# Optimization experiments

Measured on AMD Instinct MI355X. Metric: run time of the kernel, lower is better.

The kernel has to match this reference:

```python
import jax, jax.numpy as jnp
import numpy as np
import math

B, L, H = 32, 2048, 8
DMET, SDIM = 16, 27
DM, NL, DS, TE = 256, 4, 64, 256
LT = L + H - 1
DT_MIN, DT_MAX = 1e-3, 0.1


def setup_inputs() -> dict:
    key = jax.random.key(0)
    ks = jax.random.split(key, 24)
    inp = {
        'x_past': jax.random.normal(ks[0], (B, L, DMET), jnp.float32),
        'noisy_future': jax.random.normal(ks[1], (B, H, 1), jnp.float32),
        't': jax.random.uniform(ks[2], (B,), jnp.float32),
        'x_future': jax.random.normal(ks[3], (B, H - 1, DMET), jnp.float32),
        'static_attr': jax.random.normal(ks[4], (B, 1, SDIM), jnp.float32),
        # MPFourier buffers
        'freqs': 2 * math.pi * jax.random.normal(ks[5], (TE,), jnp.float32),
        'phases': 2 * math.pi * jax.random.uniform(ks[6], (TE,), jnp.float32),
        # input projection (d_met+1+static_dim -> d_model)
        'in_W': jax.random.normal(ks[7], (DMET + 1 + SDIM, DM), jnp.float32) / np.sqrt(DMET + 1 + SDIM),
        'in_b': jnp.zeros((DM,), jnp.float32),
        # time MLP
        'tm_W1': jax.random.normal(ks[8], (TE, 2 * TE), jnp.float32) / np.sqrt(TE),
        'tm_b1': jnp.zeros((2 * TE,), jnp.float32),
        'tm_W2': jax.random.normal(ks[9], (2 * TE, DM), jnp.float32) / np.sqrt(2 * TE),
        'tm_b2': jnp.zeros((DM,), jnp.float32),
        # stacked S4D (LTI) block params, leading dim = n_layers
        'log_dt': jax.random.uniform(ks[10], (NL, DM), jnp.float32) * (math.log(DT_MAX) - math.log(DT_MIN)) + math.log(DT_MIN),
        'A_re': -0.5 * jnp.ones((NL, DM, DS), jnp.float32),
        'A_im': math.pi * jnp.broadcast_to(jnp.arange(DS, dtype=jnp.float32), (NL, DM, DS)),
        'C_re': jax.random.normal(ks[11], (NL, DM, DS), jnp.float32) * (0.5 ** 0.5),
        'C_im': jax.random.normal(ks[12], (NL, DM, DS), jnp.float32) * (0.5 ** 0.5),
        'D': jax.random.normal(ks[13], (NL, DM), jnp.float32),
        'out_W': jax.random.normal(ks[14], (NL, DM, 2 * DM), jnp.float32) / np.sqrt(DM),
        'out_b': jnp.zeros((NL, 2 * DM), jnp.float32),
        # batchnorm
        'bn_gamma': jnp.ones((NL, DM), jnp.float32),
        'bn_beta': jnp.zeros((NL, DM), jnp.float32),
        # head
        'head_W1': jax.random.normal(ks[15], (DM, DM // 2), jnp.float32) / np.sqrt(DM),
        'head_b1': jnp.zeros((DM // 2,), jnp.float32),
        'head_W2': jax.random.normal(ks[16], (DM // 2, 1), jnp.float32) / np.sqrt(DM // 2),
        'head_b2': jnp.zeros((1,), jnp.float32),
    }
    return inp


def _ssm_block(u, log_dt, A_re, A_im, C_re, C_im, D, out_W, out_b):
    # u: [B, d, Lc]. S4D-style diagonal SSM via FFT causal convolution.
    Lc = u.shape[-1]
    dt = jnp.exp(log_dt)                                 # [d]
    A = A_re + 1j * A_im                                 # [d, n], Re(A) < 0
    dtA = dt[:, None] * A                                # [d, n]
    Ck = (C_re + 1j * C_im) * jnp.expm1(dtA) / A         # ZOH-style discretized C
    van = jnp.exp(dtA[:, :, None] * jnp.arange(Lc))      # [d, n, Lc] Vandermonde
    K = 2.0 * jnp.einsum('dn,dnl->dl', Ck, van).real     # [d, Lc]
    nfft = 2 * Lc
    y = jnp.fft.irfft(jnp.fft.rfft(u, nfft) * jnp.fft.rfft(K, nfft)[None], nfft)[..., :Lc]
    y = jax.nn.gelu(y + D[None, :, None] * u)
    z = jnp.einsum('bdl,de->bel', y, out_W) + out_b[None, :, None]  # [B, 2d, Lc]
    z1, z2 = jnp.split(z, 2, axis=1)
    return z1 * jax.nn.sigmoid(z2)                       # GLU


def _batchnorm1d(h, gamma, beta):
    # h: [B, d, Lc]; training-mode batch statistics, eps matches torch default.
    mean = h.mean(axis=(0, 2), keepdims=True)
    var = ((h - mean) ** 2).mean(axis=(0, 2), keepdims=True)
    return (h - mean) * jax.lax.rsqrt(var + 1e-5) * gamma[None, :, None] + beta[None, :, None]


def reference(x_past, noisy_future, t, x_future, static_attr,
              freqs, phases, in_W, in_b, tm_W1, tm_b1, tm_W2, tm_b2,
              log_dt, A_re, A_im, C_re, C_im, D, out_W, out_b,
              bn_gamma, bn_beta, head_W1, head_b1, head_W2, head_b2):
    Bc = x_past.shape[0]
    # MPFourier time features
    t_feats = jnp.cos(t[:, None] * freqs[None, :] + phases[None, :]) * math.sqrt(2)
    t_b = jax.nn.silu(t_feats @ tm_W1 + tm_b1) @ tm_W2 + tm_b2     # [B, DM]
    # feature fusion
    all_met = jnp.concatenate([x_past, x_future], axis=1)          # [B, LT, DMET]
    all_flow = jnp.concatenate([jnp.zeros((Bc, L - 1, 1), x_past.dtype), noisy_future], axis=1)
    static_seq = jnp.broadcast_to(static_attr[:, :1, :], (Bc, LT, SDIM))
    feats = jnp.concatenate([all_met, all_flow, static_seq], axis=-1)
    h = feats @ in_W + in_b                                        # [B, LT, DM]
    h = h.at[:, L - 1:, :].add(t_b[:, None, :])                    # time_full conditioning
    h = jnp.transpose(h, (0, 2, 1))                                # [B, DM, LT]
    for i in range(NL):
        z = _ssm_block(h, log_dt[i], A_re[i], A_im[i], C_re[i], C_im[i],
                       D[i], out_W[i], out_b[i])
        h = _batchnorm1d(h + z, bn_gamma[i], bn_beta[i])           # dropout = identity (eval)
    h = jnp.transpose(h, (0, 2, 1))                                # [B, LT, DM]
    out = jax.nn.silu(h @ head_W1 + head_b1) @ head_W2 + head_b2   # [B, LT, 1]
    return out[:, -H:, :]
```

## Files before the change

### kernel.cpp

```cpp
#include <hip/hip_runtime.h>
#include <hip/hip_bf16.h>
#include <math.h>

#define B_   32
#define L_   2048
#define H_   8
#define DMET 16
#define SDIM 27
#define DM   256
#define NL   4
#define DS   64
#define TE   256
#define LT   2055
#define LTR  2176
#define TCH  128
#define NC   17
#define COLS 544
#define NTOT (B_ * LT)

typedef __attribute__((ext_vector_type(8))) short short8;
typedef __attribute__((ext_vector_type(4))) short short4v;
typedef __attribute__((ext_vector_type(4))) float floatx4;

__device__ __forceinline__ float sigmoidf_(float x) {
    float e = __builtin_amdgcn_exp2f(-1.4426950408889634f * x);
    return __builtin_amdgcn_rcpf(1.0f + e);
}

__device__ __forceinline__ float gelu_tanh(float x) {
    float inner = 1.5957691216057308f * fmaf(0.044715f * x * x, x, x);
    return x * sigmoidf_(inner);
}

__device__ __forceinline__ short bfs(float x) {
    __hip_bfloat16 h = __float2bfloat16(x);
    return *(short*)&h;
}

__device__ __forceinline__ float sbf(short s) {
    unsigned u = ((unsigned)(unsigned short)s) << 16;
    return __uint_as_float(u);
}

__device__ __forceinline__ void glds16(const void* g, void* l) {
    __builtin_amdgcn_global_load_lds(
        (const __attribute__((address_space(1))) unsigned*)g,
        (__attribute__((address_space(3))) unsigned*)l, 16, 0, 0);
}

__global__ __launch_bounds__(256) void time_mlp_kernel(
    const float* __restrict__ t, const float* __restrict__ freqs,
    const float* __restrict__ phases,
    const float* __restrict__ W1, const float* __restrict__ b1,
    const float* __restrict__ W2, const float* __restrict__ b2,
    float* __restrict__ tb) {
    int b = blockIdx.x;
    int tid = threadIdx.x;
    __shared__ float f[TE];
    __shared__ float hid[2 * TE];
    float tv = t[b];
    f[tid] = cosf(fmaf(tv, freqs[tid], phases[tid])) * 1.4142135623730951f;
    __syncthreads();
    float a0 = b1[tid], a1 = b1[tid + TE];
    for (int k = 0; k < TE; ++k) {
        float fk = f[k];
        a0 = fmaf(fk, W1[k * 2 * TE + tid], a0);
        a1 = fmaf(fk, W1[k * 2 * TE + tid + TE], a1);
    }
    hid[tid]      = a0 * sigmoidf_(a0);
    hid[tid + TE] = a1 * sigmoidf_(a1);
    __syncthreads();
    float acc = b2[tid];
    for (int j = 0; j < 2 * TE; ++j)
        acc = fmaf(hid[j], W2[j * DM + tid], acc);
    tb[b * DM + tid] = acc;
}

__global__ __launch_bounds__(256) void wt_prep_kernel(
    const float* __restrict__ out_W, __hip_bfloat16* __restrict__ Wtp) {
    int bid = blockIdx.x;
    int layer = bid >> 8, k = bid & 255;
    int e = threadIdx.x;
    const float* src = out_W + ((size_t)layer * 256 + k) * 512;
    #pragma unroll
    for (int q = 0; q < 2; ++q) {
        int ee = e + q * 256;
        int P = ee & 255, half = ee >> 8;
        int by = P >> 6, pp = P & 63;
        int g = pp >> 5;
        int tcol = (pp & 31) + half * 32;
        int c = by * 128 + g * 64 + tcol;
        Wtp[((size_t)layer * 512 + c) * 256 + k] = __float2bfloat16(src[ee]);
    }
}

__global__ __launch_bounds__(256) void input_proj_kernel(
    const float* __restrict__ xp, const float* __restrict__ nf,
    const float* __restrict__ xf, const float* __restrict__ sa,
    const float* __restrict__ inW, const float* __restrict__ inb,
    const float* __restrict__ tb, __hip_bfloat16* __restrict__ Ub) {
    int b  = blockIdx.y;
    int l0 = blockIdx.x * 256;
    int tx = threadIdx.x;
    int l  = l0 + tx;

    __shared__ float feats[256][18];
    __shared__ float Ws[17][DM];
    __shared__ float sdot[DM];
    __shared__ float tbs[DM];
    __shared__ float sstat[SDIM];

    if (tx < SDIM) sstat[tx] = sa[b * SDIM + tx];
    for (int k = 0; k < 17; ++k) Ws[k][tx] = inW[k * DM + tx];
    tbs[tx] = tb[b * DM + tx];

    bool valid = (l < LT);
    if (valid) {
        const float* src = (l < L_) ? &xp[((size_t)b * L_ + l) * DMET]
                                    : &xf[((size_t)b * (H_ - 1) + (l - L_)) * DMET];
        #pragma unroll
        for (int k = 0; k < DMET; ++k) feats[tx][k] = src[k];
        feats[tx][16] = (l >= L_ - 1) ? nf[b * H_ + (l - (L_ - 1))] : 0.0f;
    }
    __syncthreads();

    float sd = 0.0f;
    for (int k = 0; k < SDIM; ++k)
        sd = fmaf(sstat[k], inW[(17 + k) * DM + tx], sd);
    sdot[tx] = sd;
    __syncthreads();

    if (l >= LTR) return;
    size_t baseb = ((size_t)b * DM) * LTR + l;
    if (!valid) {
        __hip_bfloat16 z = __float2bfloat16(0.0f);
        for (int d = 0; d < DM; ++d) Ub[baseb + (size_t)d * LTR] = z;
        return;
    }
    bool cond = (l >= L_ - 1);
    for (int d = 0; d < DM; ++d) {
        float acc = inb[d] + sdot[d] + (cond ? tbs[d] : 0.0f);
        #pragma unroll
        for (int k = 0; k < 17; ++k)
            acc = fmaf(feats[tx][k], Ws[k][d], acc);
        Ub[baseb + (size_t)d * LTR] = __float2bfloat16(acc);
    }
}

__global__ __launch_bounds__(256) void prep_kernel(
    const float* __restrict__ log_dt,
    const float* __restrict__ A_re, const float* __restrict__ A_im,
    const float* __restrict__ C_re, const float* __restrict__ C_im,
    const float* __restrict__ Dp,
    const float* __restrict__ gamma, const float* __restrict__ beta,
    float* __restrict__ stats, float* __restrict__ scsh,
    __hip_bfloat16* __restrict__ Abig, __hip_bfloat16* __restrict__ SA,
    float* __restrict__ Rsh, float* __restrict__ T1sh, int layer) {
    int d = blockIdx.x;
    int t = threadIdx.x;
    __shared__ float sAr[64], sAi[64], sCkr[64], sCki[64];
    __shared__ float kap[TCH];
    __shared__ float csum[TCH];
    __shared__ float s_sc, s_sh;

    if (t == 0) {
        float sc, sh;
        if (layer == 0) { sc = 1.0f; sh = 0.0f; }
        else {
            float s = stats[d], q = stats[DM + d];
            float mean = s * (1.0f / NTOT);
            float var  = q * (1.0f / NTOT) - mean * mean;
            sc = rsqrtf(var + 1e-5f) * gamma[(layer - 1) * DM + d];
            sh = beta[(layer - 1) * DM + d] - mean * sc;
        }
        s_sc = sc; s_sh = sh;
        scsh[d] = sc; scsh[DM + d] = sh;
        stats[d] = 0.0f; stats[DM + d] = 0.0f;
    }
    __syncthreads();
    float sc = s_sc, sh = s_sh;

    float dt = expf(log_dt[layer * DM + d]);
    float Dd = Dp[layer * DM + d];
    if (t < 64) {
        size_t ab = ((size_t)layer * DM + d) * DS + t;
        float Ar = A_re[ab], Ai = A_im[ab], Cr = C_re[ab], Ci = C_im[ab];
        float ar = dt * Ar, ai = dt * Ai;
        float e = expf(ar);
        float wre = e * cosf(ai), wim = e * sinf(ai);
        float mr = wre - 1.0f, mi = wim;
        float den = 1.0f / (Ar * Ar + Ai * Ai);
        float qr = (mr * Ar + mi * Ai) * den, qi = (mi * Ar - mr * Ai) * den;
        sCkr[t] = Cr * qr - Ci * qi;
        sCki[t] = Cr * qi + Ci * qr;
        sAr[t] = ar;
        sAi[t] = ai;
        float s2 = sinf(0.5f * ai);
        float dr = fmaf(expm1f(ar), cosf(ai), -2.0f * s2 * s2);
        float di = e * sinf(ai);
        float a128 = 128.0f * ar, b128 = 128.0f * ai;
        float s2b = sinf(0.5f * b128);
        float nr = fmaf(expm1f(a128), cosf(b128), -2.0f * s2b * s2b);
        float ni = expf(a128) * sinf(b128);
        float dd2 = 1.0f / (dr * dr + di * di);
        float gr = (nr * dr + ni * di) * dd2;
        float gi = (ni * dr - nr * di) * dd2;
        Rsh[(size_t)d * 128 + t]      = sh * gr;
        Rsh[(size_t)d * 128 + 64 + t] = sh * gi;
    }
    __syncthreads();

    {
        int delta = t >> 1, half = t & 1;
        float fd = (float)delta;
        float p = 0.0f;
        #pragma unroll 8
        for (int n = half * 32; n < half * 32 + 32; ++n) {
            float er = expf(fd * sAr[n]);
            float ph = fd * sAi[n];
            p += er * (sCkr[n] * cosf(ph) - sCki[n] * sinf(ph));
        }
        p += __shfl_xor(p, 1);
        if (half == 0) kap[delta] = 2.0f * p + (delta == 0 ? Dd : 0.0f);
    }
    __syncthreads();

    if (t < 128) csum[t] = kap[t];
    __syncthreads();
    for (int off = 1; off < 128; off <<= 1) {
        float v = 0.0f;
        if (t >= off && t < 128) v = csum[t - off];
        __syncthreads();
        if (t < 128) csum[t] += v;
        __syncthreads();
    }
    if (t < 128) T1sh[(size_t)d * 128 + t] = sh * csum[t];

    __hip_bfloat16* Ad = Abig + (size_t)d * TCH * 256;
    for (int idx = t; idx < TCH * TCH; idx += 256) {
        int i = idx >> 7, m = idx & 127;
        Ad[(size_t)i * 256 + m] = __float2bfloat16(m <= i ? sc * kap[i - m] : 0.0f);
    }
    for (int idx = t; idx < TCH * 64; idx += 256) {
        int i = idx >> 6, n = idx & 63;
        float fp = (float)(i + 1);
        float er = expf(fp * sAr[n]);
        float ph = fp * sAi[n];
        float c = cosf(ph), s = sinf(ph);
        float vr = er * (sCkr[n] * c - sCki[n] * s);
        float vi = er * (sCkr[n] * s + sCki[n] * c);
        Ad[(size_t)i * 256 + 128 + n] = __float2bfloat16(2.0f * vr);
        Ad[(size_t)i * 256 + 192 + n] = __float2bfloat16(-2.0f * vi);
    }
    __hip_bfloat16* Sd = SA + (size_t)d * TCH * TCH;
    for (int idx = t; idx < 64 * TCH; idx += 256) {
        int n = idx >> 7, m = idx & 127;
        float fp = (float)(127 - m);
        float er = sc * expf(fp * sAr[n]);
        float ph = fp * sAi[n];
        Sd[(size_t)n * 128 + m]        = __float2bfloat16(er * cosf(ph));
        Sd[(size_t)(64 + n) * 128 + m] = __float2bfloat16(er * sinf(ph));
    }
}

__global__ __launch_bounds__(256) void sgemm_kernel(
    const __hip_bfloat16* __restrict__ Ub, const __hip_bfloat16* __restrict__ SA,
    const float* __restrict__ Rsh, __hip_bfloat16* __restrict__ S) {
    int id = blockIdx.x;
    int xcd = id & 7, j = id >> 3;
    int d = xcd * 32 + ((j * 7282) >> 16);
    int cb = j - ((j * 7282) >> 16) * 9;
    int tid = threadIdx.x, wave = tid >> 6, lane = tid & 63;
    int lm = lane & 15, quad = lane >> 4;
    const __hip_bfloat16* SAd = SA + (size_t)d * TCH * TCH;

    __shared__ short Bs[8192];

    short8 a0r[4], a1r[4];
    #pragma unroll
    for (int kk = 0; kk < 4; ++kk) {
        a0r[kk] = *(const short8*)(SAd + (size_t)(wave * 32 + lm) * TCH + kk * 32 + quad * 8);
        a1r[kk] = *(const short8*)(SAd + (size_t)(wave * 32 + 16 + lm) * TCH + kk * 32 + quad * 8);
    }

    #pragma unroll
    for (int it = 0; it < 4; ++it) {
        int idx = it * 256 + tid;
        int kk = idx >> 8;
        int nt = (idx >> 6) & 3;
        int q  = (idx >> 4) & 3;
        int cc = idx & 15;
        int col = cb * 64 + nt * 16 + cc;
        int colc = col < COLS ? col : COLS - 1;
        int bh = (colc * 241) >> 12;
        int c = colc - bh * 17;
        const __hip_bfloat16* src =
            Ub + ((size_t)bh * DM + d) * LTR + (size_t)c * TCH + kk * 32 + q * 8;
        glds16(src, (char*)Bs + idx * 16);
    }

    floatx4 acc[2][4];
    floatx4 zf = {0.f, 0.f, 0.f, 0.f};
    #pragma unroll
    for (int mi = 0; mi < 2; ++mi)
        #pragma unroll
        for (int nt = 0; nt < 4; ++nt) acc[mi][nt] = zf;

    asm volatile("s_waitcnt vmcnt(2)" ::: "memory");
    __builtin_amdgcn_s_barrier();
    asm volatile("" ::: "memory");

    #pragma unroll
    for (int kk = 0; kk < 2; ++kk) {
        #pragma unroll
        for (int nt = 0; nt < 4; ++nt) {
            short8 bv = *(const short8*)(Bs + kk * 2048 + nt * 512 + lane * 8);
            acc[0][nt] = __builtin_amdgcn_mfma_f32_16x16x32_bf16(a0r[kk], bv, acc[0][nt], 0, 0, 0);
            acc[1][nt] = __builtin_amdgcn_mfma_f32_16x16x32_bf16(a1r[kk], bv, acc[1][nt], 0, 0, 0);
        }
    }

    asm volatile("s_waitcnt vmcnt(0)" ::: "memory");
    __builtin_amdgcn_s_barrier();
    asm volatile("" ::: "memory");

    #pragma unroll
    for (int kk = 2; kk < 4; ++kk) {
        #pragma unroll
        for (int nt = 0; nt < 4; ++nt) {
            short8 bv = *(const short8*)(Bs + kk * 2048 + nt * 512 + lane * 8);
            acc[0][nt] = __builtin_amdgcn_mfma_f32_16x16x32_bf16(a0r[kk], bv, acc[0][nt], 0, 0, 0);
            acc[1][nt] = __builtin_amdgcn_mfma_f32_16x16x32_bf16(a1r[kk], bv, acc[1][nt], 0, 0, 0);
        }
    }

    #pragma unroll
    for (int mi = 0; mi < 2; ++mi) {
        int row = wave * 32 + mi * 16 + quad * 4;
        float4 rs = *(const float4*)(Rsh + (size_t)d * 128 + row);
        #pragma unroll
        for (int nt = 0; nt < 4; ++nt) {
            int col = cb * 64 + nt * 16 + lm;
            if (col >= COLS) continue;
            short4v o;
            o[0] = bfs(acc[mi][nt][0] + rs.x); o[1] = bfs(acc[mi][nt][1] + rs.y);
            o[2] = bfs(acc[mi][nt][2] + rs.z); o[3] = bfs(acc[mi][nt][3] + rs.w);
            *(short4v*)(S + ((size_t)d * COLS + col) * TCH + row) = o;
        }
    }
}

__global__ __launch_bounds__(64) void carry_kernel(
    __hip_bfloat16* __restrict__ SX,
    const float* __restrict__ log_dt,
    const float* __restrict__ A_re, const float* __restrict__ A_im,
    int layer) {
    int d = blockIdx.x, b = blockIdx.y;
    int n = threadIdx.x;
    float dt = expf(log_dt[layer * DM + d]);
    size_t ab = ((size_t)layer * DM + d) * DS + n;
    float Ar = A_re[ab], Ai = A_im[ab];
    float e = expf(dt * Ar);
    float wre = e * cosf(dt * Ai), wim = e * sinf(dt * Ai);
    #pragma unroll
    for (int t = 0; t < 7; ++t) {
        float r = wre * wre - wim * wim;
        wim = 2.0f * wre * wim; wre = r;
    }
    size_t base = ((size_t)d * COLS + (size_t)b * NC) * TCH + n;
    float sre[NC], sim[NC];
    #pragma unroll
    for (int c = 0; c < NC; ++c) {
        sre[c] = __bfloat162float(SX[base + (size_t)c * TCH]);
        sim[c] = __bfloat162float(SX[base + (size_t)c * TCH + 64]);
    }
    float xr = 0.0f, xi = 0.0f;
    #pragma unroll
    for (int c = 0; c < NC; ++c) {
        SX[base + (size_t)c * TCH]      = __float2bfloat16(xr);
        SX[base + (size_t)c * TCH + 64] = __float2bfloat16(xi);
        float nr = wre * xr - wim * xi + sre[c];
        xi = wre * xi + wim * xr + sim[c];
        xr = nr;
    }
}

__global__ __launch_bounds__(256) void mainscan_kernel(
    const __hip_bfloat16* __restrict__ Ub, const __hip_bfloat16* __restrict__ X,
    const __hip_bfloat16* __restrict__ Abig, const float* __restrict__ T1sh,
    __hip_bfloat16* __restrict__ Ybt) {
    int id = blockIdx.x;
    int xcd = id & 7, j = id >> 3;
    int d = xcd * 32 + ((j * 7282) >> 16);
    int cb = j - ((j * 7282) >> 16) * 9;
    int tid = threadIdx.x, wave = tid >> 6, lane = tid & 63;
    int lm = lane & 15, quad = lane >> 4;
    const __hip_bfloat16* Ad = Abig + (size_t)d * TCH * 256;

    __shared__ short Bs[16384];

    short8 a0r[8], a1r[8];
    #pragma unroll
    for (int kk = 0; kk < 8; ++kk) {
        a0r[kk] = *(const short8*)(Ad + (size_t)(wave * 32 + lm) * 256 + kk * 32 + quad * 8);
        a1r[kk] = *(const short8*)(Ad + (size_t)(wave * 32 + 16 + lm) * 256 + kk * 32 + quad * 8);
    }

    #pragma unroll
    for (int it = 0; it < 8; ++it) {
        int idx = it * 256 + tid;
        int kk = idx >> 8;
        int nt = (idx >> 6) & 3;
        int q  = (idx >> 4) & 3;
        int cc = idx & 15;
        int col = cb * 64 + nt * 16 + cc;
        int colc = col < COLS ? col : COLS - 1;
        int bh = (colc * 241) >> 12;
        int c = colc - bh * 17;
        const __hip_bfloat16* src;
        if (kk < 4)
            src = Ub + ((size_t)bh * DM + d) * LTR + (size_t)c * TCH + kk * 32 + q * 8;
        else
            src = X + ((size_t)d * COLS + colc) * TCH + (kk - 4) * 32 + q * 8;
        glds16(src, (char*)Bs + idx * 16);
    }

    floatx4 acc[2][4];
    floatx4 zf = {0.f, 0.f, 0.f, 0.f};
    #pragma unroll
    for (int mi = 0; mi < 2; ++mi)
        #pragma unroll
        for (int nt = 0; nt < 4; ++nt) acc[mi][nt] = zf;

    asm volatile("s_waitcnt vmcnt(4)" ::: "memory");
    __builtin_amdgcn_s_barrier();
    asm volatile("" ::: "memory");

    #pragma unroll
    for (int kk = 0; kk < 4; ++kk) {
        #pragma unroll
        for (int nt = 0; nt < 4; ++nt) {
            short8 bv = *(const short8*)(Bs + kk * 2048 + nt * 512 + lane * 8);
            acc[0][nt] = __builtin_amdgcn_mfma_f32_16x16x32_bf16(a0r[kk], bv, acc[0][nt], 0, 0, 0);
            acc[1][nt] = __builtin_amdgcn_mfma_f32_16x16x32_bf16(a1r[kk], bv, acc[1][nt], 0, 0, 0);
        }
    }

    asm volatile("s_waitcnt vmcnt(0)" ::: "memory");
    __builtin_amdgcn_s_barrier();
    asm volatile("" ::: "memory");

    #pragma unroll
    for (int kk = 4; kk < 8; ++kk) {
        #pragma unroll
        for (int nt = 0; nt < 4; ++nt) {
            short8 bv = *(const short8*)(Bs + kk * 2048 + nt * 512 + lane * 8);
            acc[0][nt] = __builtin_amdgcn_mfma_f32_16x16x32_bf16(a0r[kk], bv, acc[0][nt], 0, 0, 0);
            acc[1][nt] = __builtin_amdgcn_mfma_f32_16x16x32_bf16(a1r[kk], bv, acc[1][nt], 0, 0, 0);
        }
    }

    #pragma unroll
    for (int mi = 0; mi < 2; ++mi) {
        int row0 = wave * 32 + mi * 16 + quad * 4;
        float4 t1 = *(const float4*)(T1sh + (size_t)d * 128 + row0);
        #pragma unroll
        for (int nt = 0; nt < 4; ++nt) {
            int col = cb * 64 + nt * 16 + lm;
            if (col >= COLS) continue;
            int bh = (col * 241) >> 12;
            int c = col - bh * 17;
            int l0 = c * TCH + row0;
            float g0 = gelu_tanh(acc[mi][nt][0] + t1.x);
            float g1 = gelu_tanh(acc[mi][nt][1] + t1.y);
            float g2 = gelu_tanh(acc[mi][nt][2] + t1.z);
            float g3 = gelu_tanh(acc[mi][nt][3] + t1.w);
            __hip_bfloat16* dst = Ybt + ((size_t)bh * DM + d) * LTR + l0;
            if (l0 + 3 < LT) {
                short4v o;
                o[0] = bfs(g0); o[1] = bfs(g1); o[2] = bfs(g2); o[3] = bfs(g3);
                *(short4v*)dst = o;
            } else {
                if (l0 + 0 < LT) dst[0] = __float2bfloat16(g0);
                if (l0 + 1 < LT) dst[1] = __float2bfloat16(g1);
                if (l0 + 2 < LT) dst[2] = __float2bfloat16(g2);
                if (l0 + 3 < LT) dst[3] = __float2bfloat16(g3);
            }
        }
    }
}

__global__ __launch_bounds__(256) void gemm_glu_mfma_kernel(
    const __hip_bfloat16* __restrict__ Ybt, __hip_bfloat16* __restrict__ Ub,
    const __hip_bfloat16* __restrict__ Wtp, const float* __restrict__ out_b,
    const float* __restrict__ scsh, float* __restrict__ stats, int layer) {
    int id = blockIdx.x;
    int r8 = id & 7, j = id >> 3;
    int by = r8 >> 1;
    int sub = (r8 & 1) * 272 + j;
    int bq = (sub * 3856) >> 16;
    int bx = sub - bq * 17;
    int b = bq;
    int tid = threadIdx.x;
    int wave = tid >> 6, lane = tid & 63;
    int lm = lane & 15, quad = lane >> 4;
    int l0 = bx * 128;

    __shared__ short lds[16384];

    const __hip_bfloat16* Wl = Wtp + (size_t)layer * 512 * 256 + (size_t)by * 128 * 256;

    int kp = tid >> 4;
    int l8 = tid & 15;
    const __hip_bfloat16* srcA = Ybt + ((size_t)b * DM + 2 * kp) * LTR + l0 + l8 * 8;
    int woff[8];
    {
        int qA = kp >> 2;
        #pragma unroll
        for (int jj = 0; jj < 8; ++jj) {
            int lloc = l8 * 8 + jj;
            int s4 = (qA + lloc + l8) & 3;
            woff[jj] = lloc * 32 + s4 * 8 + (kp & 3) * 2;
        }
    }
    int rB_[2], qB_[2];
    #pragma unroll
    for (int i = 0; i < 2; ++i) {
        int u = i * 256 + tid;
        int r = u >> 2;
        rB_[i] = r;
        qB_[i] = ((u & 3) - r - (r >> 3)) & 3;
    }
    int aoff[4], boff[4];
    #pragma unroll
    for (int mi = 0; mi < 4; ++mi) {
        int r = (wave >> 1) * 64 + mi * 16 + lm;
        aoff[mi] = r * 32 + ((quad + r + (r >> 3)) & 3) * 8;
    }
    #pragma unroll
    for (int ni = 0; ni < 4; ++ni) {
        int r = (wave & 1) * 64 + ni * 16 + lm;
        boff[ni] = r * 32 + ((quad + r + (r >> 3)) & 3) * 8;
    }

    floatx4 acc[4][4];
    floatx4 zf = {0.f, 0.f, 0.f, 0.f};
    #pragma unroll
    for (int mi = 0; mi < 4; ++mi)
        #pragma unroll
        for (int ni = 0; ni < 4; ++ni) acc[mi][ni] = zf;

#define STAGE_B(S, P)                                                         \
    {                                                                         \
        char* bb_ = (char*)(lds + (P) * 8192 + 4096);                         \
        _Pragma("unroll")                                                     \
        for (int i_ = 0; i_ < 2; ++i_)                                        \
            glds16(Wl + (size_t)rB_[i_] * 256 + (S) * 32 + qB_[i_] * 8,       \
                   bb_ + (i_ * 256 + tid) * 16);                              \
    }
#define LOAD_A(S, G0, G1)                                                     \
    {                                                                         \
        const __hip_bfloat16* pa_ = srcA + (size_t)(S) * 32 * LTR;            \
        G0 = *(const short8*)pa_;                                             \
        G1 = *(const short8*)(pa_ + LTR);                                     \
    }
#define WRITE_A(P, G0, G1)                                                    \
    {                                                                         \
        short* ab_ = lds + (P) * 8192;                                        \
        _Pragma("unroll")                                                     \
        for (int j_ = 0; j_ < 8; ++j_) {                                      \
            unsigned pk_ = (unsigned)(unsigned short)G0[j_] |                 \
                           ((unsigned)(unsigned short)G1[j_] << 16);          \
            *(unsigned*)(ab_ + woff[j_]) = pk_;                               \
        }                                                                     \
    }
#define COMPUTE(P)                                                            \
    {                                                                         \
        const short* ab_ = lds + (P) * 8192;                                  \
        const short* bb_ = ab_ + 4096;                                        \
        short8 af_[4], bf_[4];                                                \
        _Pragma("unroll")                                                     \
        for (int mi_ = 0; mi_ < 4; ++mi_)                                     \
            af_[mi_] = *(const short8*)(ab_ + aoff[mi_]);                     \
        _Pragma("unroll")                                                     \
        for (int ni_ = 0; ni_ < 4; ++ni_)                                     \
            bf_[ni_] = *(const short8*)(bb_ + boff[ni_]);                     \
        _Pragma("unroll")                                                     \
        for (int mi_ = 0; mi_ < 4; ++mi_)                                     \
            _Pragma("unroll")                                                 \
            for (int ni_ = 0; ni_ < 4; ++ni_)                                 \
                acc[mi_][ni_] = __builtin_amdgcn_mfma_f32_16x16x32_bf16(      \
                    af_[mi_], bf_[ni_], acc[mi_][ni_], 0, 0, 0);              \
    }
#define FENCE2                                                                \
    asm volatile("s_waitcnt vmcnt(2)" ::: "memory");                          \
    asm volatile("s_waitcnt lgkmcnt(0)" ::: "memory");                        \
    __builtin_amdgcn_sched_barrier(0);                                        \
    __builtin_amdgcn_s_barrier();
#define FENCE0                                                                \
    asm volatile("s_waitcnt vmcnt(0)" ::: "memory");                          \
    asm volatile("s_waitcnt lgkmcnt(0)" ::: "memory");                        \
    __builtin_amdgcn_sched_barrier(0);                                        \
    __builtin_amdgcn_s_barrier();

    short8 gE0, gE1, gO0, gO1;
    STAGE_B(0, 0);
    LOAD_A(0, gE0, gE1);
    WRITE_A(0, gE0, gE1);
    LOAD_A(1, gO0, gO1);
    asm volatile("s_waitcnt lgkmcnt(0)" ::: "memory");
    __builtin_amdgcn_sched_barrier(0);
    __builtin_amdgcn_s_barrier();

    STAGE_B(1, 1); COMPUTE(0); WRITE_A(1, gO0, gO1); LOAD_A(2, gE0, gE1); FENCE2;
    STAGE_B(2, 0); COMPUTE(1); WRITE_A(0, gE0, gE1); LOAD_A(3, gO0, gO1); FENCE2;
    STAGE_B(3, 1); COMPUTE(0); WRITE_A(1, gO0, gO1); LOAD_A(4, gE0, gE1); FENCE2;
    STAGE_B(4, 0); COMPUTE(1); WRITE_A(0, gE0, gE1); LOAD_A(5, gO0, gO1); FENCE2;
    STAGE_B(5, 1); COMPUTE(0); WRITE_A(1, gO0, gO1); LOAD_A(6, gE0, gE1); FENCE2;
    STAGE_B(6, 0); COMPUTE(1); WRITE_A(0, gE0, gE1); LOAD_A(7, gO0, gO1); FENCE2;
    STAGE_B(7, 1); COMPUTE(0); WRITE_A(1, gO0, gO1); FENCE0;
    COMPUTE(1);

#undef STAGE_B
#undef LOAD_A
#undef WRITE_A
#undef COMPUTE
#undef FENCE2
#undef FENCE0

    const float* bl = out_b + layer * 512;
    int Pbase = by * 64 + (wave & 1) * 32;
    int lw = l0 + (wave >> 1) * 64;
    #pragma unroll
    for (int ni = 0; ni < 2; ++ni) {
        int P = Pbase + ni * 16 + lm;
        float bz1 = bl[P], bz2 = bl[256 + P];
        float scP = scsh[P], shP = scsh[DM + P];
        __hip_bfloat16* ubrow = Ub + ((size_t)b * DM + P) * LTR;
        float sp = 0.f, sq = 0.f;
        #pragma unroll
        for (int mi = 0; mi < 4; ++mi) {
            int l0q = lw + mi * 16 + quad * 4;
            if (l0q >= LT) continue;
            floatx4 z1 = acc[mi][ni];
            floatx4 z2 = acc[mi][ni + 2];
            if (l0q + 4 <= LT) {
                short4v uv = *(const short4v*)(ubrow + l0q);
                float h0 = fmaf(scP, sbf(uv[0]), shP) + (z1[0] + bz1) * sigmoidf_(z2[0] + bz2);
                float h1 = fmaf(scP, sbf(uv[1]), shP) + (z1[1] + bz1) * sigmoidf_(z2[1] + bz2);
                float h2 = fmaf(scP, sbf(uv[2]), shP) + (z1[2] + bz1) * sigmoidf_(z2[2] + bz2);
                float h3 = fmaf(scP, sbf(uv[3]), shP) + (z1[3] + bz1) * sigmoidf_(z2[3] + bz2);
                short4v ov;
                ov[0] = bfs(h0); ov[1] = bfs(h1); ov[2] = bfs(h2); ov[3] = bfs(h3);
                *(short4v*)(ubrow + l0q) = ov;
                sp += (h0 + h1) + (h2 + h3);
                sq += (h0 * h0 + h1 * h1) + (h2 * h2 + h3 * h3);
            } else {
                #pragma unroll
                for (int r = 0; r < 4; ++r) {
                    int l = l0q + r;
                    if (l < LT) {
                        float uvv = __bfloat162float(ubrow[l]);
                        float hh = fmaf(scP, uvv, shP) + (z1[r] + bz1) * sigmoidf_(z2[r] + bz2);
                        ubrow[l] = __float2bfloat16(hh);
                        sp += hh; sq += hh * hh;
                    }
                }
            }
        }
        sp += __shfl_xor(sp, 16); sp += __shfl_xor(sp, 32);
        sq += __shfl_xor(sq, 16); sq += __shfl_xor(sq, 32);
        if (quad == 0) {
            atomicAdd(&stats[P], sp);
            atomicAdd(&stats[DM + P], sq);
        }
    }
}

__global__ __launch_bounds__(256) void statsfin_kernel(
    const float* __restrict__ stats,
    const float* __restrict__ gamma, const float* __restrict__ beta,
    float* __restrict__ scsh, int layer) {
    int d = threadIdx.x;
    float s = stats[d], q = stats[DM + d];
    float mean = s * (1.0f / NTOT);
    float var  = q * (1.0f / NTOT) - mean * mean;
    float sc = rsqrtf(var + 1e-5f) * gamma[layer * DM + d];
    scsh[d] = sc;
    scsh[DM + d] = beta[layer * DM + d] - mean * sc;
}

__global__ __launch_bounds__(128) void head_kernel(
    const __hip_bfloat16* __restrict__ Ub, const float* __restrict__ scsh,
    const float* __restrict__ W1, const float* __restrict__ b1,
    const float* __restrict__ W2, const float* __restrict__ b2,
    float* __restrict__ out) {
    int hh = blockIdx.x;
    int b  = blockIdx.y;
    int j  = threadIdx.x;
    int l  = (L_ - 1) + hh;
    const __hip_bfloat16* urow = Ub + ((size_t)b * DM) * LTR + l;
    float a = b1[j];
    for (int k = 0; k < DM; ++k) {
        float hn = fmaf(scsh[k], __bfloat162float(urow[(size_t)k * LTR]), scsh[DM + k]);
        a = fmaf(hn, W1[k * 128 + j], a);
    }
    float hs = a * sigmoidf_(a);
    float v = hs * W2[j];
    v += __shfl_xor(v, 1);
    v += __shfl_xor(v, 2);
    v += __shfl_xor(v, 4);
    v += __shfl_xor(v, 8);
    v += __shfl_xor(v, 16);
    v += __shfl_xor(v, 32);
    __shared__ float partial[2];
    if ((j & 63) == 0) partial[j >> 6] = v;
    __syncthreads();
    if (j == 0) out[b * H_ + hh] = partial[0] + partial[1] + b2[0];
}

extern "C" void kernel_launch(void* const* d_in, const int* in_sizes, int n_in,
                              void* d_out, int out_size, void* d_ws, size_t ws_size,
                              hipStream_t stream) {
    (void)in_sizes; (void)n_in; (void)out_size; (void)ws_size;
    const float* x_past      = (const float*)d_in[0];
    const float* noisy       = (const float*)d_in[1];
    const float* t_in        = (const float*)d_in[2];
    const float* x_future    = (const float*)d_in[3];
    const float* static_attr = (const float*)d_in[4];
    const float* freqs       = (const float*)d_in[5];
    const float* phases      = (const float*)d_in[6];
    const float* in_W        = (const float*)d_in[7];
    const float* in_b        = (const float*)d_in[8];
    const float* tm_W1       = (const float*)d_in[9];
    const float* tm_b1       = (const float*)d_in[10];
    const float* tm_W2       = (const float*)d_in[11];
    const float* tm_b2       = (const float*)d_in[12];
    const float* log_dt      = (const float*)d_in[13];
    const float* A_re        = (const float*)d_in[14];
    const float* A_im        = (const float*)d_in[15];
    const float* C_re        = (const float*)d_in[16];
    const float* C_im        = (const float*)d_in[17];
    const float* Dp          = (const float*)d_in[18];
    const float* out_W       = (const float*)d_in[19];
    const float* out_b       = (const float*)d_in[20];
    const float* bn_gamma    = (const float*)d_in[21];
    const float* bn_beta     = (const float*)d_in[22];
    const float* head_W1     = (const float*)d_in[23];
    const float* head_b1     = (const float*)d_in[24];
    const float* head_W2     = (const float*)d_in[25];
    const float* head_b2     = (const float*)d_in[26];

    char* ws = (char*)d_ws;
    const size_t UB_OFF = 1u << 20;
    const size_t UB_BYT = (size_t)B_ * DM * LTR * 2;
    const size_t R1_OFF = UB_OFF + UB_BYT;
    const size_t RB     = (size_t)256 * COLS * TCH * 2;
    const size_t R2_OFF = R1_OFF + RB;
    const size_t AB_OFF = R2_OFF + RB;
    const size_t AB_BYT = (size_t)256 * TCH * 256 * 2;
    const size_t SA_OFF = AB_OFF + AB_BYT;
    const size_t SA_BYT = (size_t)256 * TCH * TCH * 2;
    const size_t WT_OFF = SA_OFF + SA_BYT;

    float*          tb    = (float*)(ws);
    float*          stats = (float*)(ws + (64 << 10));
    float*          scsh  = (float*)(ws + (96 << 10));
    float*          Rsh   = (float*)(ws + (128 << 10));
    float*          T1sh  = (float*)(ws + (256 << 10));
    __hip_bfloat16* Ub    = (__hip_bfloat16*)(ws + UB_OFF);
    __hip_bfloat16* R1    = (__hip_bfloat16*)(ws + R1_OFF);
    __hip_bfloat16* Ybt   = (__hip_bfloat16*)(ws + R2_OFF);
    __hip_bfloat16* Abig  = (__hip_bfloat16*)(ws + AB_OFF);
    __hip_bfloat16* SA    = (__hip_bfloat16*)(ws + SA_OFF);
    __hip_bfloat16* Wtp   = (__hip_bfloat16*)(ws + WT_OFF);

    time_mlp_kernel<<<dim3(B_), 256, 0, stream>>>(
        t_in, freqs, phases, tm_W1, tm_b1, tm_W2, tm_b2, tb);

    wt_prep_kernel<<<dim3(NL * 256), 256, 0, stream>>>(out_W, Wtp);

    input_proj_kernel<<<dim3(9, B_), 256, 0, stream>>>(
        x_past, noisy, x_future, static_attr, in_W, in_b, tb, Ub);

    for (int layer = 0; layer < NL; ++layer) {
        prep_kernel<<<dim3(256), 256, 0, stream>>>(
            log_dt, A_re, A_im, C_re, C_im, Dp, bn_gamma, bn_beta,
            stats, scsh, Abig, SA, Rsh, T1sh, layer);
        sgemm_kernel<<<dim3(2304), 256, 0, stream>>>(Ub, SA, Rsh, R1);
        carry_kernel<<<dim3(256, B_), 64, 0, stream>>>(
            R1, log_dt, A_re, A_im, layer);
        mainscan_kernel<<<dim3(2304), 256, 0, stream>>>(Ub, R1, Abig, T1sh, Ybt);
        gemm_glu_mfma_kernel<<<dim3(2176), 256, 0, stream>>>(
            Ybt, Ub, Wtp, out_b, scsh, stats, layer);
    }

    statsfin_kernel<<<dim3(1), 256, 0, stream>>>(
        stats, bn_gamma, bn_beta, scsh, NL - 1);

    head_kernel<<<dim3(H_, B_), 128, 0, stream>>>(
        Ub, scsh, head_W1, head_b1, head_W2, head_b2, (float*)d_out);
}
```

Baseline: 840.5 us.

## Process three column tiles per block with pipelined LDS staging in scan GEMMs

sgemm and mainscan now have each block handle three 64-column tiles instead of one, cutting the grid from 2304 to 768 blocks. The register-resident A fragments are reused across the three tiles, and a triple-buffered LDS ring lets the global-to-LDS loads for the next tile overlap the MFMA work and epilogue of the current one. The prep kernel also switches to hardware exp2/sin/cos intrinsics with manual range reduction, which is less accurate than the libm calls. More LDS per block and fewer blocks may lower occupancy and parallelism across the CUs.

```diff
diff --git a/kernel.cpp b/kernel.cpp
--- a/kernel.cpp
+++ b/kernel.cpp
@@ -32,6 +32,20 @@
     return x * sigmoidf_(inner);
 }
 
+__device__ __forceinline__ float fexp_(float x) {
+    return __builtin_amdgcn_exp2f(1.4426950408889634f * x);
+}
+__device__ __forceinline__ float fsin_(float ph) {
+    float r = ph * 0.15915494309189535f;
+    r = r - floorf(r);
+    return __builtin_amdgcn_sinf(r);
+}
+__device__ __forceinline__ float fcos_(float ph) {
+    float r = ph * 0.15915494309189535f;
+    r = r - floorf(r);
+    return __builtin_amdgcn_cosf(r);
+}
+
 __device__ __forceinline__ short bfs(float x) {
     __hip_bfloat16 h = __float2bfloat16(x);
     return *(short*)&h;
@@ -47,6 +61,12 @@
         (const __attribute__((address_space(1))) unsigned*)g,
         (__attribute__((address_space(3))) unsigned*)l, 16, 0, 0);
 }
+
+#define BARV(n) do {                                                          \
+    asm volatile("s_waitcnt vmcnt(" #n ") lgkmcnt(0)" ::: "memory");          \
+    __builtin_amdgcn_s_barrier();                                             \
+    asm volatile("" ::: "memory");                                            \
+} while (0)
 
 __global__ __launch_bounds__(256) void time_mlp_kernel(
     const float* __restrict__ t, const float* __restrict__ freqs,
@@ -216,9 +236,9 @@
         float p = 0.0f;
         #pragma unroll 8
         for (int n = half * 32; n < half * 32 + 32; ++n) {
-            float er = expf(fd * sAr[n]);
+            float er = fexp_(fd * sAr[n]);
             float ph = fd * sAi[n];
-            p += er * (sCkr[n] * cosf(ph) - sCki[n] * sinf(ph));
+            p += er * (sCkr[n] * fcos_(ph) - sCki[n] * fsin_(ph));
         }
         p += __shfl_xor(p, 1);
         if (half == 0) kap[delta] = 2.0f * p + (delta == 0 ? Dd : 0.0f);
@@ -244,9 +264,9 @@
     for (int idx = t; idx < TCH * 64; idx += 256) {
         int i = idx >> 6, n = idx & 63;
         float fp = (float)(i + 1);
-        float er = expf(fp * sAr[n]);
+        float er = fexp_(fp * sAr[n]);
         float ph = fp * sAi[n];
-        float c = cosf(ph), s = sinf(ph);
+        float c = fcos_(ph), s = fsin_(ph);
         float vr = er * (sCkr[n] * c - sCki[n] * s);
         float vi = er * (sCkr[n] * s + sCki[n] * c);
         Ad[(size_t)i * 256 + 128 + n] = __float2bfloat16(2.0f * vr);
@@ -256,10 +276,10 @@
     for (int idx = t; idx < 64 * TCH; idx += 256) {
         int n = idx >> 7, m = idx & 127;
         float fp = (float)(127 - m);
-        float er = sc * expf(fp * sAr[n]);
+        float er = sc * fexp_(fp * sAr[n]);
         float ph = fp * sAi[n];
-        Sd[(size_t)n * 128 + m]        = __float2bfloat16(er * cosf(ph));
-        Sd[(size_t)(64 + n) * 128 + m] = __float2bfloat16(er * sinf(ph));
+        Sd[(size_t)n * 128 + m]        = __float2bfloat16(er * fcos_(ph));
+        Sd[(size_t)(64 + n) * 128 + m] = __float2bfloat16(er * fsin_(ph));
     }
 }
 
@@ -268,13 +288,14 @@
     const float* __restrict__ Rsh, __hip_bfloat16* __restrict__ S) {
     int id = blockIdx.x;
     int xcd = id & 7, j = id >> 3;
-    int d = xcd * 32 + ((j * 7282) >> 16);
-    int cb = j - ((j * 7282) >> 16) * 9;
+    int dj = (j * 21846) >> 16;
+    int d = xcd * 32 + dj;
+    int g = j - dj * 3;
     int tid = threadIdx.x, wave = tid >> 6, lane = tid & 63;
     int lm = lane & 15, quad = lane >> 4;
     const __hip_bfloat16* SAd = SA + (size_t)d * TCH * TCH;
 
-    __shared__ short Bs[8192];
+    __shared__ short Bs[12288];
 
     short8 a0r[4], a1r[4];
     #pragma unroll
@@ -283,21 +304,19 @@
         a1r[kk] = *(const short8*)(SAd + (size_t)(wave * 32 + 16 + lm) * TCH + kk * 32 + quad * 8);
     }
 
-    #pragma unroll
-    for (int it = 0; it < 4; ++it) {
-        int idx = it * 256 + tid;
-        int kk = idx >> 8;
-        int nt = (idx >> 6) & 3;
-        int q  = (idx >> 4) & 3;
-        int cc = idx & 15;
-        int col = cb * 64 + nt * 16 + cc;
+    int ntS = (tid >> 6) & 3, qS = (tid >> 4) & 3, ccS = tid & 15;
+    const __hip_bfloat16* srcB[3];
+    #pragma unroll
+    for (int t = 0; t < 3; ++t) {
+        int col = (3 * g + t) * 64 + ntS * 16 + ccS;
         int colc = col < COLS ? col : COLS - 1;
         int bh = (colc * 241) >> 12;
         int c = colc - bh * 17;
-        const __hip_bfloat16* src =
-            Ub + ((size_t)bh * DM + d) * LTR + (size_t)c * TCH + kk * 32 + q * 8;
-        glds16(src, (char*)Bs + idx * 16);
-    }
+        srcB[t] = Ub + ((size_t)bh * DM + d) * LTR + (size_t)c * TCH + qS * 8;
+    }
+
+    float4 rs0 = *(const float4*)(Rsh + (size_t)d * 128 + wave * 32 + quad * 4);
+    float4 rs1 = *(const float4*)(Rsh + (size_t)d * 128 + wave * 32 + 16 + quad * 4);
 
     floatx4 acc[2][4];
     floatx4 zf = {0.f, 0.f, 0.f, 0.f};
@@ -306,48 +325,72 @@
         #pragma unroll
         for (int nt = 0; nt < 4; ++nt) acc[mi][nt] = zf;
 
-    asm volatile("s_waitcnt vmcnt(2)" ::: "memory");
-    __builtin_amdgcn_s_barrier();
-    asm volatile("" ::: "memory");
-
-    #pragma unroll
-    for (int kk = 0; kk < 2; ++kk) {
-        #pragma unroll
-        for (int nt = 0; nt < 4; ++nt) {
-            short8 bv = *(const short8*)(Bs + kk * 2048 + nt * 512 + lane * 8);
-            acc[0][nt] = __builtin_amdgcn_mfma_f32_16x16x32_bf16(a0r[kk], bv, acc[0][nt], 0, 0, 0);
-            acc[1][nt] = __builtin_amdgcn_mfma_f32_16x16x32_bf16(a1r[kk], bv, acc[1][nt], 0, 0, 0);
-        }
-    }
-
-    asm volatile("s_waitcnt vmcnt(0)" ::: "memory");
-    __builtin_amdgcn_s_barrier();
-    asm volatile("" ::: "memory");
-
-    #pragma unroll
-    for (int kk = 2; kk < 4; ++kk) {
-        #pragma unroll
-        for (int nt = 0; nt < 4; ++nt) {
-            short8 bv = *(const short8*)(Bs + kk * 2048 + nt * 512 + lane * 8);
-            acc[0][nt] = __builtin_amdgcn_mfma_f32_16x16x32_bf16(a0r[kk], bv, acc[0][nt], 0, 0, 0);
-            acc[1][nt] = __builtin_amdgcn_mfma_f32_16x16x32_bf16(a1r[kk], bv, acc[1][nt], 0, 0, 0);
-        }
-    }
-
-    #pragma unroll
-    for (int mi = 0; mi < 2; ++mi) {
-        int row = wave * 32 + mi * 16 + quad * 4;
-        float4 rs = *(const float4*)(Rsh + (size_t)d * 128 + row);
-        #pragma unroll
-        for (int nt = 0; nt < 4; ++nt) {
-            int col = cb * 64 + nt * 16 + lm;
-            if (col >= COLS) continue;
-            short4v o;
-            o[0] = bfs(acc[mi][nt][0] + rs.x); o[1] = bfs(acc[mi][nt][1] + rs.y);
-            o[2] = bfs(acc[mi][nt][2] + rs.z); o[3] = bfs(acc[mi][nt][3] + rs.w);
-            *(short4v*)(S + ((size_t)d * COLS + col) * TCH + row) = o;
-        }
-    }
+#define SG_STAGE(t_, kk0_, off_)                                              \
+    {                                                                         \
+        glds16(srcB[t_] + (kk0_) * 32,     (char*)Bs + (off_) + tid * 16);    \
+        glds16(srcB[t_] + (kk0_ + 1) * 32, (char*)Bs + (off_) + 4096 + tid * 16); \
+    }
+#define SG_COMP(off_, kkA_)                                                   \
+    {                                                                         \
+        const short* bb_ = (const short*)((const char*)Bs + (off_));          \
+        _Pragma("unroll")                                                     \
+        for (int kk_ = 0; kk_ < 2; ++kk_) {                                   \
+            _Pragma("unroll")                                                 \
+            for (int nt_ = 0; nt_ < 4; ++nt_) {                               \
+                short8 bv = *(const short8*)(bb_ + kk_ * 2048 + nt_ * 512 + lane * 8); \
+                acc[0][nt_] = __builtin_amdgcn_mfma_f32_16x16x32_bf16(        \
+                    a0r[(kkA_) + kk_], bv, acc[0][nt_], 0, 0, 0);             \
+                acc[1][nt_] = __builtin_amdgcn_mfma_f32_16x16x32_bf16(        \
+                    a1r[(kkA_) + kk_], bv, acc[1][nt_], 0, 0, 0);             \
+            }                                                                 \
+        }                                                                     \
+    }
+#define SG_EPI(cb_)                                                           \
+    _Pragma("unroll")                                                         \
+    for (int mi = 0; mi < 2; ++mi) {                                          \
+        int row = wave * 32 + mi * 16 + quad * 4;                             \
+        float4 rs = mi ? rs1 : rs0;                                           \
+        _Pragma("unroll")                                                     \
+        for (int nt_ = 0; nt_ < 4; ++nt_) {                                   \
+            int col = (cb_) * 64 + nt_ * 16 + lm;                             \
+            if (col < COLS) {                                                 \
+                short4v o;                                                    \
+                o[0] = bfs(acc[mi][nt_][0] + rs.x);                           \
+                o[1] = bfs(acc[mi][nt_][1] + rs.y);                           \
+                o[2] = bfs(acc[mi][nt_][2] + rs.z);                           \
+                o[3] = bfs(acc[mi][nt_][3] + rs.w);                           \
+                *(short4v*)(S + ((size_t)d * COLS + col) * TCH + row) = o;    \
+            }                                                                 \
+            acc[mi][nt_] = zf;                                                \
+        }                                                                     \
+    }
+
+    SG_STAGE(0, 0, 0);
+    SG_STAGE(0, 2, 8192);
+    SG_STAGE(1, 0, 16384);
+    BARV(4);
+    SG_COMP(0, 0);
+    BARV(2);
+    SG_STAGE(1, 2, 0);
+    SG_COMP(8192, 2);
+    BARV(2);
+    SG_STAGE(2, 0, 8192);
+    SG_EPI(3 * g + 0);
+    BARV(4);
+    SG_COMP(16384, 0);
+    BARV(2);
+    SG_STAGE(2, 2, 16384);
+    SG_COMP(0, 2);
+    SG_EPI(3 * g + 1);
+    BARV(2);
+    SG_COMP(8192, 0);
+    BARV(0);
+    SG_COMP(16384, 2);
+    SG_EPI(3 * g + 2);
+
+#undef SG_STAGE
+#undef SG_COMP
+#undef SG_EPI
 }
 
 __global__ __launch_bounds__(64) void carry_kernel(
@@ -391,13 +434,14 @@
     __hip_bfloat16* __restrict__ Ybt) {
     int id = blockIdx.x;
     int xcd = id & 7, j = id >> 3;
-    int d = xcd * 32 + ((j * 7282) >> 16);
-    int cb = j - ((j * 7282) >> 16) * 9;
+    int dj = (j * 21846) >> 16;
+    int d = xcd * 32 + dj;
+    int g = j - dj * 3;
     int tid = threadIdx.x, wave = tid >> 6, lane = tid & 63;
     int lm = lane & 15, quad = lane >> 4;
     const __hip_bfloat16* Ad = Abig + (size_t)d * TCH * 256;
 
-    __shared__ short Bs[16384];
+    __shared__ short Bs[24576];
 
     short8 a0r[8], a1r[8];
     #pragma unroll
@@ -406,24 +450,21 @@
         a1r[kk] = *(const short8*)(Ad + (size_t)(wave * 32 + 16 + lm) * 256 + kk * 32 + quad * 8);
     }
 
-    #pragma unroll
-    for (int it = 0; it < 8; ++it) {
-        int idx = it * 256 + tid;
-        int kk = idx >> 8;
-        int nt = (idx >> 6) & 3;
-        int q  = (idx >> 4) & 3;
-        int cc = idx & 15;
-        int col = cb * 64 + nt * 16 + cc;
+    int ntS = (tid >> 6) & 3, qS = (tid >> 4) & 3, ccS = tid & 15;
+    const __hip_bfloat16* srcU[3];
+    const __hip_bfloat16* srcX[3];
+    #pragma unroll
+    for (int t = 0; t < 3; ++t) {
+        int col = (3 * g + t) * 64 + ntS * 16 + ccS;
         int colc = col < COLS ? col : COLS - 1;
         int bh = (colc * 241) >> 12;
         int c = colc - bh * 17;
-        const __hip_bfloat16* src;
-        if (kk < 4)
-            src = Ub + ((size_t)bh * DM + d) * LTR + (size_t)c * TCH + kk * 32 + q * 8;
-        else
-            src = X + ((size_t)d * COLS + colc) * TCH + (kk - 4) * 32 + q * 8;
-        glds16(src, (char*)Bs + idx * 16);
-    }
+        srcU[t] = Ub + ((size_t)bh * DM + d) * LTR + (size_t)c * TCH + qS * 8;
+        srcX[t] = X + ((size_t)d * COLS + colc) * TCH + qS * 8;
+    }
+
+    float4 t1a = *(const float4*)(T1sh + (size_t)d * 128 + wave * 32 + quad * 4);
+    float4 t1b = *(const float4*)(T1sh + (size_t)d * 128 + wave * 32 + 16 + quad * 4);
 
     floatx4 acc[2][4];
     floatx4 zf = {0.f, 0.f, 0.f, 0.f};
@@ -432,62 +473,95 @@
         #pragma unroll
         for (int nt = 0; nt < 4; ++nt) acc[mi][nt] = zf;
 
-    asm volatile("s_waitcnt vmcnt(4)" ::: "memory");
-    __builtin_amdgcn_s_barrier();
-    asm volatile("" ::: "memory");
-
-    #pragma unroll
-    for (int kk = 0; kk < 4; ++kk) {
-        #pragma unroll
-        for (int nt = 0; nt < 4; ++nt) {
-            short8 bv = *(const short8*)(Bs + kk * 2048 + nt * 512 + lane * 8);
-            acc[0][nt] = __builtin_amdgcn_mfma_f32_16x16x32_bf16(a0r[kk], bv, acc[0][nt], 0, 0, 0);
-            acc[1][nt] = __builtin_amdgcn_mfma_f32_16x16x32_bf16(a1r[kk], bv, acc[1][nt], 0, 0, 0);
-        }
-    }
-
-    asm volatile("s_waitcnt vmcnt(0)" ::: "memory");
-    __builtin_amdgcn_s_barrier();
-    asm volatile("" ::: "memory");
-
-    #pragma unroll
-    for (int kk = 4; kk < 8; ++kk) {
-        #pragma unroll
-        for (int nt = 0; nt < 4; ++nt) {
-            short8 bv = *(const short8*)(Bs + kk * 2048 + nt * 512 + lane * 8);
-            acc[0][nt] = __builtin_amdgcn_mfma_f32_16x16x32_bf16(a0r[kk], bv, acc[0][nt], 0, 0, 0);
-            acc[1][nt] = __builtin_amdgcn_mfma_f32_16x16x32_bf16(a1r[kk], bv, acc[1][nt], 0, 0, 0);
-        }
-    }
-
-    #pragma unroll
-    for (int mi = 0; mi < 2; ++mi) {
-        int row0 = wave * 32 + mi * 16 + quad * 4;
-        float4 t1 = *(const float4*)(T1sh + (size_t)d * 128 + row0);
-        #pragma unroll
-        for (int nt = 0; nt < 4; ++nt) {
-            int col = cb * 64 + nt * 16 + lm;
-            if (col >= COLS) continue;
-            int bh = (col * 241) >> 12;
-            int c = col - bh * 17;
-            int l0 = c * TCH + row0;
-            float g0 = gelu_tanh(acc[mi][nt][0] + t1.x);
-            float g1 = gelu_tanh(acc[mi][nt][1] + t1.y);
-            float g2 = gelu_tanh(acc[mi][nt][2] + t1.z);
-            float g3 = gelu_tanh(acc[mi][nt][3] + t1.w);
-            __hip_bfloat16* dst = Ybt + ((size_t)bh * DM + d) * LTR + l0;
-            if (l0 + 3 < LT) {
-                short4v o;
-                o[0] = bfs(g0); o[1] = bfs(g1); o[2] = bfs(g2); o[3] = bfs(g3);
-                *(short4v*)dst = o;
-            } else {
-                if (l0 + 0 < LT) dst[0] = __float2bfloat16(g0);
-                if (l0 + 1 < LT) dst[1] = __float2bfloat16(g1);
-                if (l0 + 2 < LT) dst[2] = __float2bfloat16(g2);
-                if (l0 + 3 < LT) dst[3] = __float2bfloat16(g3);
-            }
-        }
-    }
+#define MS_STAGE_LO(t_, off_)                                                 \
+    {                                                                         \
+        _Pragma("unroll")                                                     \
+        for (int k_ = 0; k_ < 4; ++k_)                                        \
+            glds16(srcU[t_] + k_ * 32,                                        \
+                   (char*)Bs + (off_) + k_ * 4096 + tid * 16);                \
+    }
+#define MS_STAGE_HI(t_, off_)                                                 \
+    {                                                                         \
+        _Pragma("unroll")                                                     \
+        for (int k_ = 0; k_ < 4; ++k_)                                        \
+            glds16(srcX[t_] + k_ * 32,                                        \
+                   (char*)Bs + (off_) + k_ * 4096 + tid * 16);                \
+    }
+#define MS_COMP(off_, kkA_)                                                   \
+    {                                                                         \
+        const short* bb_ = (const short*)((const char*)Bs + (off_));          \
+        _Pragma("unroll")                                                     \
+        for (int kk_ = 0; kk_ < 4; ++kk_) {                                   \
+            _Pragma("unroll")                                                 \
+            for (int nt_ = 0; nt_ < 4; ++nt_) {                               \
+                short8 bv = *(const short8*)(bb_ + kk_ * 2048 + nt_ * 512 + lane * 8); \
+                acc[0][nt_] = __builtin_amdgcn_mfma_f32_16x16x32_bf16(        \
+                    a0r[(kkA_) + kk_], bv, acc[0][nt_], 0, 0, 0);             \
+                acc[1][nt_] = __builtin_amdgcn_mfma_f32_16x16x32_bf16(        \
+                    a1r[(kkA_) + kk_], bv, acc[1][nt_], 0, 0, 0);             \
+            }                                                                 \
+        }                                                                     \
+    }
+#define MS_EPI(cb_)                                                           \
+    _Pragma("unroll")                                                         \
+    for (int mi = 0; mi < 2; ++mi) {                                          \
+        int row0 = wave * 32 + mi * 16 + quad * 4;                            \
+        float4 t1 = mi ? t1b : t1a;                                           \
+        _Pragma("unroll")                                                     \
+        for (int nt_ = 0; nt_ < 4; ++nt_) {                                   \
+            int col = (cb_) * 64 + nt_ * 16 + lm;                             \
+            if (col < COLS) {                                                 \
+                int bh = (col * 241) >> 12;                                   \
+                int c = col - bh * 17;                                        \
+                int l0 = c * TCH + row0;                                      \
+                float g0 = gelu_tanh(acc[mi][nt_][0] + t1.x);                 \
+                float g1 = gelu_tanh(acc[mi][nt_][1] + t1.y);                 \
+                float g2 = gelu_tanh(acc[mi][nt_][2] + t1.z);                 \
+                float g3 = gelu_tanh(acc[mi][nt_][3] + t1.w);                 \
+                __hip_bfloat16* dst = Ybt + ((size_t)bh * DM + d) * LTR + l0; \
+                if (l0 + 3 < LT) {                                            \
+                    short4v o;                                                \
+                    o[0] = bfs(g0); o[1] = bfs(g1);                           \
+                    o[2] = bfs(g2); o[3] = bfs(g3);                           \
+                    *(short4v*)dst = o;                                       \
+                } else {                                                      \
+                    if (l0 + 0 < LT) dst[0] = __float2bfloat16(g0);           \
+                    if (l0 + 1 < LT) dst[1] = __float2bfloat16(g1);           \
+                    if (l0 + 2 < LT) dst[2] = __float2bfloat16(g2);           \
+                    if (l0 + 3 < LT) dst[3] = __float2bfloat16(g3);           \
+                }                                                             \
+            }                                                                 \
+            acc[mi][nt_] = zf;                                                \
+        }                                                                     \
+    }
+
+    MS_STAGE_LO(0, 0);
+    MS_STAGE_HI(0, 16384);
+    MS_STAGE_LO(1, 32768);
+    BARV(8);
+    MS_COMP(0, 0);
+    BARV(4);
+    MS_STAGE_HI(1, 0);
+    MS_COMP(16384, 4);
+    BARV(4);
+    MS_STAGE_LO(2, 16384);
+    MS_EPI(3 * g + 0);
+    BARV(8);
+    MS_COMP(32768, 0);
+    BARV(4);
+    MS_STAGE_HI(2, 32768);
+    MS_COMP(0, 4);
+    MS_EPI(3 * g + 1);
+    BARV(4);
+    MS_COMP(16384, 0);
+    BARV(0);
+    MS_COMP(32768, 4);
+    MS_EPI(3 * g + 2);
+
+#undef MS_STAGE_LO
+#undef MS_STAGE_HI
+#undef MS_COMP
+#undef MS_EPI
 }
 
 __global__ __launch_bounds__(256) void gemm_glu_mfma_kernel(
@@ -787,10 +861,10 @@
         prep_kernel<<<dim3(256), 256, 0, stream>>>(
             log_dt, A_re, A_im, C_re, C_im, Dp, bn_gamma, bn_beta,
             stats, scsh, Abig, SA, Rsh, T1sh, layer);
-        sgemm_kernel<<<dim3(2304), 256, 0, stream>>>(Ub, SA, Rsh, R1);
+        sgemm_kernel<<<dim3(768), 256, 0, stream>>>(Ub, SA, Rsh, R1);
         carry_kernel<<<dim3(256, B_), 64, 0, stream>>>(
             R1, log_dt, A_re, A_im, layer);
-        mainscan_kernel<<<dim3(2304), 256, 0, stream>>>(Ub, R1, Abig, T1sh, Ybt);
+        mainscan_kernel<<<dim3(768), 256, 0, stream>>>(Ub, R1, Abig, T1sh, Ybt);
         gemm_glu_mfma_kernel<<<dim3(2176), 256, 0, stream>>>(
             Ybt, Ub, Wtp, out_b, scsh, stats, layer);
     }
```

Measured after the change: 703.5 us. 16.3% less time.
